# Performance work log

Hardware: AMD Instinct MI355X
Metric: run time of the kernel (lower is better)

## Reference

```python
import jax, jax.numpy as jnp
import numpy as np

N = 1_000_000   # gaussians
K_NB = 10       # neighbor control points per gaussian
K_TOTAL = 300   # num_fine control points


def _normalize(q, eps=1e-8):
    return q / jnp.maximum(jnp.linalg.norm(q, axis=-1, keepdims=True), eps)


def quaternion_to_rotation_matrix(q):
    # q: [..., 4] in (w, x, y, z); normalized before conversion
    q = _normalize(q)
    w, x, y, z = q[..., 0], q[..., 1], q[..., 2], q[..., 3]
    R = jnp.stack([
        jnp.stack([1 - 2 * (y * y + z * z), 2 * (x * y - w * z), 2 * (x * z + w * y)], axis=-1),
        jnp.stack([2 * (x * y + w * z), 1 - 2 * (x * x + z * z), 2 * (y * z - w * x)], axis=-1),
        jnp.stack([2 * (x * z - w * y), 2 * (y * z + w * x), 1 - 2 * (x * x + y * y)], axis=-1),
    ], axis=-2)  # [..., 3, 3]
    return R


def quaternion_multiply(a, b):
    # Hamilton product, (w, x, y, z)
    aw, ax, ay, az = a[..., 0], a[..., 1], a[..., 2], a[..., 3]
    bw, bx, by, bz = b[..., 0], b[..., 1], b[..., 2], b[..., 3]
    return jnp.stack([
        aw * bw - ax * bx - ay * by - az * bz,
        aw * bx + ax * bw + ay * bz - az * by,
        aw * by - ax * bz + ay * bw + az * bx,
        aw * bz + ax * by - ay * bx + az * bw,
    ], axis=-1)


def setup_inputs() -> dict:
    key = jax.random.key(0)
    ks = jax.random.split(key, 7)
    means = jax.random.normal(ks[0], (N, 3), dtype=jnp.float32)
    quaternions = _normalize(jax.random.normal(ks[1], (N, 4), dtype=jnp.float32))
    w = jax.random.uniform(ks[2], (N, K_NB), dtype=jnp.float32) + 1e-3
    weights = w / w.sum(-1, keepdims=True)  # blending weights sum to 1
    indices = jax.random.randint(ks[3], (N, K_NB), 0, K_TOTAL)
    ctrl_translations = 0.1 * jax.random.normal(ks[4], (K_TOTAL, 3), dtype=jnp.float32)
    ctrl_rotations = _normalize(jax.random.normal(ks[5], (K_TOTAL, 4), dtype=jnp.float32))
    ctrl_positions = jax.random.normal(ks[6], (K_TOTAL, 3), dtype=jnp.float32)
    return {
        'means': means, 'quaternions': quaternions, 'weights': weights,
        'ctrl_translations': ctrl_translations, 'ctrl_rotations': ctrl_rotations,
        'ctrl_positions': ctrl_positions, 'indices': indices,
    }


def reference(means, quaternions, weights, ctrl_translations, ctrl_rotations, ctrl_positions, indices):
    # gather neighbor control-point transforms
    nb_trans = ctrl_translations[indices]   # [N, K, 3]
    nb_rots = ctrl_rotations[indices]       # [N, K, 4]
    nb_pos = ctrl_positions[indices]        # [N, K, 3]

    diff = means[:, None, :] - nb_pos                       # [N, K, 3]
    R_ctrl = quaternion_to_rotation_matrix(nb_rots)         # [N, K, 3, 3]
    rotated_diff = jnp.einsum('nkij,nkj->nki', R_ctrl, diff)
    deformed_per_cp = rotated_diff + nb_pos + nb_trans      # [N, K, 3]

    w = weights[..., None]                                  # [N, K, 1]
    deformed_means = (w * deformed_per_cp).sum(axis=1)      # [N, 3]

    blended_rot = _normalize((w * nb_rots).sum(axis=1))     # [N, 4]
    deformed_quats = quaternion_multiply(blended_rot, quaternions)
    return deformed_means, deformed_quats
```

## Files before the change

kernel.cpp:

```cpp
#include <hip/hip_runtime.h>
#include <math.h>


__device__ __forceinline__ void compute_cp(
    const float* __restrict__ ctrl_trans,
    const float* __restrict__ ctrl_rot,
    const float* __restrict__ ctrl_pos,
    int cp, float4* q_out, float4* b_out)
{
    float qw = ctrl_rot[cp * 4 + 0];
    float qx = ctrl_rot[cp * 4 + 1];
    float qy = ctrl_rot[cp * 4 + 2];
    float qz = ctrl_rot[cp * 4 + 3];
    float n   = sqrtf(qw * qw + qx * qx + qy * qy + qz * qz);
    float inv = 1.0f / fmaxf(n, 1e-8f);
    float w = qw * inv, x = qx * inv, y = qy * inv, z = qz * inv;
    float R00 = 1.0f - 2.0f * (y * y + z * z);
    float R01 = 2.0f * (x * y - w * z);
    float R02 = 2.0f * (x * z + w * y);
    float R10 = 2.0f * (x * y + w * z);
    float R11 = 1.0f - 2.0f * (x * x + z * z);
    float R12 = 2.0f * (y * z - w * x);
    float R20 = 2.0f * (x * z - w * y);
    float R21 = 2.0f * (y * z + w * x);
    float R22 = 1.0f - 2.0f * (x * x + y * y);
    float px = ctrl_pos[cp * 3 + 0];
    float py = ctrl_pos[cp * 3 + 1];
    float pz = ctrl_pos[cp * 3 + 2];
    float tx = ctrl_trans[cp * 3 + 0];
    float ty = ctrl_trans[cp * 3 + 1];
    float tz = ctrl_trans[cp * 3 + 2];
    *q_out = make_float4(w, x, y, z);
    *b_out = make_float4(px + tx - (R00 * px + R01 * py + R02 * pz),
                         py + ty - (R10 * px + R11 * py + R12 * pz),
                         pz + tz - (R20 * px + R21 * py + R22 * pz),
                         0.0f);
}

__global__ __launch_bounds__(256) void build_table_kernel(
    const float* __restrict__ ctrl_trans,
    const float* __restrict__ ctrl_rot,
    const float* __restrict__ ctrl_pos,
    float4* __restrict__ table, int K_TOTAL)
{
    int cp = blockIdx.x * blockDim.x + threadIdx.x;
    if (cp >= K_TOTAL) return;
    float4 q, b;
    compute_cp(ctrl_trans, ctrl_rot, ctrl_pos, cp, &q, &b);
    table[cp] = q;
    table[K_TOTAL + cp] = b;
}

template <int KNB>
__device__ __forceinline__ void deform_body(
    const float4* __restrict__ s4,
    const float* __restrict__ means,
    const float* __restrict__ quats,
    const float* __restrict__ weights,
    const int*   __restrict__ indices,
    float* __restrict__ out_means,
    float* __restrict__ out_quats,
    int i, int K_TOTAL, int K_NB_rt)
{
    const int kn = (KNB > 0) ? KNB : K_NB_rt;
    const int*   idx_row = indices + (long long)i * kn;
    const float* w_row   = weights + (long long)i * kn;

    float W = 0.0f;
    float Mxx = 0.0f, Myy = 0.0f, Mzz = 0.0f;
    float Mxy = 0.0f, Mxz = 0.0f, Myz = 0.0f;
    float Mwx = 0.0f, Mwy = 0.0f, Mwz = 0.0f;
    float qsw = 0.0f, qsx = 0.0f, qsy = 0.0f, qsz = 0.0f;
    float bsx = 0.0f, bsy = 0.0f, bsz = 0.0f;

#pragma unroll
    for (int k = 0; k < kn; k++) {
        int   cp = idx_row[k];
        float w  = w_row[k];
        float4 q = s4[cp];
        float4 b = s4[K_TOTAL + cp];
        float tw = w * q.x, tx = w * q.y, ty = w * q.z, tz = w * q.w;
        W += w;
        Mxx = fmaf(tx, q.y, Mxx);
        Myy = fmaf(ty, q.z, Myy);
        Mzz = fmaf(tz, q.w, Mzz);
        Mxy = fmaf(tx, q.z, Mxy);
        Mxz = fmaf(tx, q.w, Mxz);
        Myz = fmaf(ty, q.w, Myz);
        Mwx = fmaf(tw, q.y, Mwx);
        Mwy = fmaf(tw, q.z, Mwy);
        Mwz = fmaf(tw, q.w, Mwz);
        qsw += tw; qsx += tx; qsy += ty; qsz += tz;
        bsx = fmaf(w, b.x, bsx);
        bsy = fmaf(w, b.y, bsy);
        bsz = fmaf(w, b.z, bsz);
    }

    float mx = means[i * 3 + 0];
    float my = means[i * 3 + 1];
    float mz = means[i * 3 + 2];

    float A00 = W - 2.0f * (Myy + Mzz);
    float A01 = 2.0f * (Mxy - Mwz);
    float A02 = 2.0f * (Mxz + Mwy);
    float A10 = 2.0f * (Mxy + Mwz);
    float A11 = W - 2.0f * (Mxx + Mzz);
    float A12 = 2.0f * (Myz - Mwx);
    float A20 = 2.0f * (Mxz - Mwy);
    float A21 = 2.0f * (Myz + Mwx);
    float A22 = W - 2.0f * (Mxx + Myy);

    out_means[i * 3 + 0] = fmaf(A00, mx, fmaf(A01, my, fmaf(A02, mz, bsx)));
    out_means[i * 3 + 1] = fmaf(A10, mx, fmaf(A11, my, fmaf(A12, mz, bsy)));
    out_means[i * 3 + 2] = fmaf(A20, mx, fmaf(A21, my, fmaf(A22, mz, bsz)));

    float n   = sqrtf(qsw * qsw + qsx * qsx + qsy * qsy + qsz * qsz);
    float inv = 1.0f / fmaxf(n, 1e-8f);
    float bw = qsw * inv, bx = qsx * inv, by = qsy * inv, bz = qsz * inv;

    float4 g = ((const float4*)quats)[i];
    float gw = g.x, gx = g.y, gy = g.z, gz = g.w;

    float ow = bw * gw - bx * gx - by * gy - bz * gz;
    float ox = bw * gx + bx * gw + by * gz - bz * gy;
    float oy = bw * gy - bx * gz + by * gw + bz * gx;
    float oz = bw * gz + bx * gy - by * gx + bz * gw;

    float4* oq = (float4*)(out_quats + (long long)i * 4);
    *oq = make_float4(ow, ox, oy, oz);
}

template <int KNB>
__global__ __launch_bounds__(256) void deform_kernel(
    const float* __restrict__ means,
    const float* __restrict__ quats,
    const float* __restrict__ weights,
    const float4* __restrict__ table,
    const int*   __restrict__ indices,
    float* __restrict__ out_means,
    float* __restrict__ out_quats,
    int N, int K_TOTAL, int K_NB_rt)
{
    extern __shared__ float4 s4[];
    int nelem = 2 * K_TOTAL;
    for (int t = threadIdx.x; t < nelem; t += blockDim.x) s4[t] = table[t];
    __syncthreads();

    int i = blockIdx.x * blockDim.x + threadIdx.x;
    if (i >= N) return;
    deform_body<KNB>(s4, means, quats, weights, indices, out_means, out_quats,
                     i, K_TOTAL, K_NB_rt);
}

template <int KNB>
__global__ __launch_bounds__(256) void deform_fused_kernel(
    const float* __restrict__ means,
    const float* __restrict__ quats,
    const float* __restrict__ weights,
    const float* __restrict__ ctrl_trans,
    const float* __restrict__ ctrl_rot,
    const float* __restrict__ ctrl_pos,
    const int*   __restrict__ indices,
    float* __restrict__ out_means,
    float* __restrict__ out_quats,
    int N, int K_TOTAL, int K_NB_rt)
{
    extern __shared__ float4 s4[];
    for (int cp = threadIdx.x; cp < K_TOTAL; cp += blockDim.x) {
        float4 q, b;
        compute_cp(ctrl_trans, ctrl_rot, ctrl_pos, cp, &q, &b);
        s4[cp] = q;
        s4[K_TOTAL + cp] = b;
    }
    __syncthreads();

    int i = blockIdx.x * blockDim.x + threadIdx.x;
    if (i >= N) return;
    deform_body<KNB>(s4, means, quats, weights, indices, out_means, out_quats,
                     i, K_TOTAL, K_NB_rt);
}

extern "C" void kernel_launch(void* const* d_in, const int* in_sizes, int n_in,
                              void* d_out, int out_size, void* d_ws, size_t ws_size,
                              hipStream_t stream) {
    const float* means      = (const float*)d_in[0];
    const float* quats      = (const float*)d_in[1];
    const float* weights    = (const float*)d_in[2];
    const float* ctrl_trans = (const float*)d_in[3];
    const float* ctrl_rot   = (const float*)d_in[4];
    const float* ctrl_pos   = (const float*)d_in[5];
    const int*   indices    = (const int*)d_in[6];

    int N       = in_sizes[0] / 3;
    int K_NB    = in_sizes[2] / N;
    int K_TOTAL = in_sizes[3] / 3;

    float* out_means = (float*)d_out;
    float* out_quats = (float*)d_out + (long long)N * 3;

    int block = 256;
    int grid  = (N + block - 1) / block;
    size_t tbl_bytes = (size_t)K_TOTAL * 2 * sizeof(float4);
    size_t smem = tbl_bytes;

    if (d_ws != nullptr && ws_size >= tbl_bytes) {
        int gb = (K_TOTAL + block - 1) / block;
        build_table_kernel<<<gb, block, 0, stream>>>(
            ctrl_trans, ctrl_rot, ctrl_pos, (float4*)d_ws, K_TOTAL);
        if (K_NB == 10) {
            deform_kernel<10><<<grid, block, smem, stream>>>(
                means, quats, weights, (const float4*)d_ws, indices,
                out_means, out_quats, N, K_TOTAL, K_NB);
        } else {
            deform_kernel<0><<<grid, block, smem, stream>>>(
                means, quats, weights, (const float4*)d_ws, indices,
                out_means, out_quats, N, K_TOTAL, K_NB);
        }
    } else {
        if (K_NB == 10) {
            deform_fused_kernel<10><<<grid, block, smem, stream>>>(
                means, quats, weights, ctrl_trans, ctrl_rot, ctrl_pos, indices,
                out_means, out_quats, N, K_TOTAL, K_NB);
        } else {
            deform_fused_kernel<0><<<grid, block, smem, stream>>>(
                means, quats, weights, ctrl_trans, ctrl_rot, ctrl_pos, indices,
                out_means, out_quats, N, K_TOTAL, K_NB);
        }
    }
}
```

Before: 147.8 us.

## Process two gaussians per thread with vectorized int4/float4 loads and fused table build

Each thread now handles a pair of gaussians, so their 20 indices and 20 weights load as five int4 and five float4 vector loads, and means and outputs use float2 and float4 accesses. The separate table-build kernel is dropped and each block computes the control-point table into shared memory itself. Table entries are interleaved so q and b for one control point sit next to each other. This aims to cut the number of memory transactions and one kernel launch. The cost is redundant per-block table setup, half as many threads in flight, and higher register use.

After: 149.4 us. Within noise of the previous version (+1.1%).

```diff
diff --git a/kernel.cpp b/kernel.cpp
--- a/kernel.cpp
+++ b/kernel.cpp
@@ -37,123 +37,74 @@
                          0.0f);
 }
 
-__global__ __launch_bounds__(256) void build_table_kernel(
-    const float* __restrict__ ctrl_trans,
-    const float* __restrict__ ctrl_rot,
-    const float* __restrict__ ctrl_pos,
-    float4* __restrict__ table, int K_TOTAL)
-{
-    int cp = blockIdx.x * blockDim.x + threadIdx.x;
-    if (cp >= K_TOTAL) return;
-    float4 q, b;
-    compute_cp(ctrl_trans, ctrl_rot, ctrl_pos, cp, &q, &b);
-    table[cp] = q;
-    table[K_TOTAL + cp] = b;
-}
-
-template <int KNB>
-__device__ __forceinline__ void deform_body(
-    const float4* __restrict__ s4,
-    const float* __restrict__ means,
-    const float* __restrict__ quats,
-    const float* __restrict__ weights,
-    const int*   __restrict__ indices,
-    float* __restrict__ out_means,
-    float* __restrict__ out_quats,
-    int i, int K_TOTAL, int K_NB_rt)
-{
-    const int kn = (KNB > 0) ? KNB : K_NB_rt;
-    const int*   idx_row = indices + (long long)i * kn;
-    const float* w_row   = weights + (long long)i * kn;
-
-    float W = 0.0f;
-    float Mxx = 0.0f, Myy = 0.0f, Mzz = 0.0f;
-    float Mxy = 0.0f, Mxz = 0.0f, Myz = 0.0f;
-    float Mwx = 0.0f, Mwy = 0.0f, Mwz = 0.0f;
-    float qsw = 0.0f, qsx = 0.0f, qsy = 0.0f, qsz = 0.0f;
-    float bsx = 0.0f, bsy = 0.0f, bsz = 0.0f;
-
-#pragma unroll
-    for (int k = 0; k < kn; k++) {
-        int   cp = idx_row[k];
-        float w  = w_row[k];
-        float4 q = s4[cp];
-        float4 b = s4[K_TOTAL + cp];
-        float tw = w * q.x, tx = w * q.y, ty = w * q.z, tz = w * q.w;
-        W += w;
-        Mxx = fmaf(tx, q.y, Mxx);
-        Myy = fmaf(ty, q.z, Myy);
-        Mzz = fmaf(tz, q.w, Mzz);
-        Mxy = fmaf(tx, q.z, Mxy);
-        Mxz = fmaf(tx, q.w, Mxz);
-        Myz = fmaf(ty, q.w, Myz);
-        Mwx = fmaf(tw, q.y, Mwx);
-        Mwy = fmaf(tw, q.z, Mwy);
-        Mwz = fmaf(tw, q.w, Mwz);
-        qsw += tw; qsx += tx; qsy += ty; qsz += tz;
-        bsx = fmaf(w, b.x, bsx);
-        bsy = fmaf(w, b.y, bsy);
-        bsz = fmaf(w, b.z, bsz);
-    }
-
-    float mx = means[i * 3 + 0];
-    float my = means[i * 3 + 1];
-    float mz = means[i * 3 + 2];
-
-    float A00 = W - 2.0f * (Myy + Mzz);
-    float A01 = 2.0f * (Mxy - Mwz);
-    float A02 = 2.0f * (Mxz + Mwy);
-    float A10 = 2.0f * (Mxy + Mwz);
-    float A11 = W - 2.0f * (Mxx + Mzz);
-    float A12 = 2.0f * (Myz - Mwx);
-    float A20 = 2.0f * (Mxz - Mwy);
-    float A21 = 2.0f * (Myz + Mwx);
-    float A22 = W - 2.0f * (Mxx + Myy);
-
-    out_means[i * 3 + 0] = fmaf(A00, mx, fmaf(A01, my, fmaf(A02, mz, bsx)));
-    out_means[i * 3 + 1] = fmaf(A10, mx, fmaf(A11, my, fmaf(A12, mz, bsy)));
-    out_means[i * 3 + 2] = fmaf(A20, mx, fmaf(A21, my, fmaf(A22, mz, bsz)));
-
-    float n   = sqrtf(qsw * qsw + qsx * qsx + qsy * qsy + qsz * qsz);
+struct Accum {
+    float W;
+    float Mxx, Myy, Mzz, Mxy, Mxz, Myz, Mwx, Mwy, Mwz;
+    float qsw, qsx, qsy, qsz;
+    float bsx, bsy, bsz;
+};
+
+__device__ __forceinline__ void acc_init(Accum& a) {
+    a.W = 0.0f;
+    a.Mxx = a.Myy = a.Mzz = 0.0f;
+    a.Mxy = a.Mxz = a.Myz = 0.0f;
+    a.Mwx = a.Mwy = a.Mwz = 0.0f;
+    a.qsw = a.qsx = a.qsy = a.qsz = 0.0f;
+    a.bsx = a.bsy = a.bsz = 0.0f;
+}
+
+__device__ __forceinline__ void acc_neighbor(Accum& a, const float4* __restrict__ s4,
+                                             int cp, float w) {
+    float4 q = s4[2 * cp];
+    float4 b = s4[2 * cp + 1];
+    float tw = w * q.x, tx = w * q.y, ty = w * q.z, tz = w * q.w;
+    a.W += w;
+    a.Mxx = fmaf(tx, q.y, a.Mxx);
+    a.Myy = fmaf(ty, q.z, a.Myy);
+    a.Mzz = fmaf(tz, q.w, a.Mzz);
+    a.Mxy = fmaf(tx, q.z, a.Mxy);
+    a.Mxz = fmaf(tx, q.w, a.Mxz);
+    a.Myz = fmaf(ty, q.w, a.Myz);
+    a.Mwx = fmaf(tw, q.y, a.Mwx);
+    a.Mwy = fmaf(tw, q.z, a.Mwy);
+    a.Mwz = fmaf(tw, q.w, a.Mwz);
+    a.qsw += tw; a.qsx += tx; a.qsy += ty; a.qsz += tz;
+    a.bsx = fmaf(w, b.x, a.bsx);
+    a.bsy = fmaf(w, b.y, a.bsy);
+    a.bsz = fmaf(w, b.z, a.bsz);
+}
+
+__device__ __forceinline__ void acc_epilogue(const Accum& a,
+                                             float mx, float my, float mz,
+                                             float4 g,
+                                             float* dmx, float* dmy, float* dmz,
+                                             float4* oq) {
+    float A00 = a.W - 2.0f * (a.Myy + a.Mzz);
+    float A01 = 2.0f * (a.Mxy - a.Mwz);
+    float A02 = 2.0f * (a.Mxz + a.Mwy);
+    float A10 = 2.0f * (a.Mxy + a.Mwz);
+    float A11 = a.W - 2.0f * (a.Mxx + a.Mzz);
+    float A12 = 2.0f * (a.Myz - a.Mwx);
+    float A20 = 2.0f * (a.Mxz - a.Mwy);
+    float A21 = 2.0f * (a.Myz + a.Mwx);
+    float A22 = a.W - 2.0f * (a.Mxx + a.Myy);
+
+    *dmx = fmaf(A00, mx, fmaf(A01, my, fmaf(A02, mz, a.bsx)));
+    *dmy = fmaf(A10, mx, fmaf(A11, my, fmaf(A12, mz, a.bsy)));
+    *dmz = fmaf(A20, mx, fmaf(A21, my, fmaf(A22, mz, a.bsz)));
+
+    float n   = sqrtf(a.qsw * a.qsw + a.qsx * a.qsx + a.qsy * a.qsy + a.qsz * a.qsz);
     float inv = 1.0f / fmaxf(n, 1e-8f);
-    float bw = qsw * inv, bx = qsx * inv, by = qsy * inv, bz = qsz * inv;
-
-    float4 g = ((const float4*)quats)[i];
+    float bw = a.qsw * inv, bx = a.qsx * inv, by = a.qsy * inv, bz = a.qsz * inv;
+
     float gw = g.x, gx = g.y, gy = g.z, gz = g.w;
-
-    float ow = bw * gw - bx * gx - by * gy - bz * gz;
-    float ox = bw * gx + bx * gw + by * gz - bz * gy;
-    float oy = bw * gy - bx * gz + by * gw + bz * gx;
-    float oz = bw * gz + bx * gy - by * gx + bz * gw;
-
-    float4* oq = (float4*)(out_quats + (long long)i * 4);
-    *oq = make_float4(ow, ox, oy, oz);
-}
-
-template <int KNB>
-__global__ __launch_bounds__(256) void deform_kernel(
-    const float* __restrict__ means,
-    const float* __restrict__ quats,
-    const float* __restrict__ weights,
-    const float4* __restrict__ table,
-    const int*   __restrict__ indices,
-    float* __restrict__ out_means,
-    float* __restrict__ out_quats,
-    int N, int K_TOTAL, int K_NB_rt)
-{
-    extern __shared__ float4 s4[];
-    int nelem = 2 * K_TOTAL;
-    for (int t = threadIdx.x; t < nelem; t += blockDim.x) s4[t] = table[t];
-    __syncthreads();
-
-    int i = blockIdx.x * blockDim.x + threadIdx.x;
-    if (i >= N) return;
-    deform_body<KNB>(s4, means, quats, weights, indices, out_means, out_quats,
-                     i, K_TOTAL, K_NB_rt);
-}
-
-template <int KNB>
-__global__ __launch_bounds__(256) void deform_fused_kernel(
+    oq->x = bw * gw - bx * gx - by * gy - bz * gz;
+    oq->y = bw * gx + bx * gw + by * gz - bz * gy;
+    oq->z = bw * gy - bx * gz + by * gw + bz * gx;
+    oq->w = bw * gz + bx * gy - by * gx + bz * gw;
+}
+
+__global__ __launch_bounds__(256) void deform_pair_kernel(
     const float* __restrict__ means,
     const float* __restrict__ quats,
     const float* __restrict__ weights,
@@ -163,21 +114,133 @@
     const int*   __restrict__ indices,
     float* __restrict__ out_means,
     float* __restrict__ out_quats,
-    int N, int K_TOTAL, int K_NB_rt)
+    int N, int K_TOTAL)
 {
     extern __shared__ float4 s4[];
     for (int cp = threadIdx.x; cp < K_TOTAL; cp += blockDim.x) {
         float4 q, b;
         compute_cp(ctrl_trans, ctrl_rot, ctrl_pos, cp, &q, &b);
-        s4[cp] = q;
-        s4[K_TOTAL + cp] = b;
+        s4[2 * cp]     = q;
+        s4[2 * cp + 1] = b;
     }
     __syncthreads();
 
-    int i = blockIdx.x * blockDim.x + threadIdx.x;
+    long long tid = (long long)blockIdx.x * blockDim.x + threadIdx.x;
+    long long i0  = 2 * tid;
+    if (i0 >= N) return;
+
+    if (i0 + 1 < N) {
+        const int4*   ip = (const int4*)(indices + i0 * 10);
+        const float4* wp = (const float4*)(weights + i0 * 10);
+        int4   I0 = ip[0], I1 = ip[1], I2 = ip[2], I3 = ip[3], I4 = ip[4];
+        float4 W0 = wp[0], W1 = wp[1], W2 = wp[2], W3 = wp[3], W4 = wp[4];
+
+        Accum a0; acc_init(a0);
+        acc_neighbor(a0, s4, I0.x, W0.x);
+        acc_neighbor(a0, s4, I0.y, W0.y);
+        acc_neighbor(a0, s4, I0.z, W0.z);
+        acc_neighbor(a0, s4, I0.w, W0.w);
+        acc_neighbor(a0, s4, I1.x, W1.x);
+        acc_neighbor(a0, s4, I1.y, W1.y);
+        acc_neighbor(a0, s4, I1.z, W1.z);
+        acc_neighbor(a0, s4, I1.w, W1.w);
+        acc_neighbor(a0, s4, I2.x, W2.x);
+        acc_neighbor(a0, s4, I2.y, W2.y);
+
+        Accum a1; acc_init(a1);
+        acc_neighbor(a1, s4, I2.z, W2.z);
+        acc_neighbor(a1, s4, I2.w, W2.w);
+        acc_neighbor(a1, s4, I3.x, W3.x);
+        acc_neighbor(a1, s4, I3.y, W3.y);
+        acc_neighbor(a1, s4, I3.z, W3.z);
+        acc_neighbor(a1, s4, I3.w, W3.w);
+        acc_neighbor(a1, s4, I4.x, W4.x);
+        acc_neighbor(a1, s4, I4.y, W4.y);
+        acc_neighbor(a1, s4, I4.z, W4.z);
+        acc_neighbor(a1, s4, I4.w, W4.w);
+
+        const float2* mp = (const float2*)(means + i0 * 3);
+        float2 m01 = mp[0], m23 = mp[1], m45 = mp[2];
+
+        float4 g0 = ((const float4*)quats)[i0];
+        float4 g1 = ((const float4*)quats)[i0 + 1];
+
+        float d0x, d0y, d0z, d1x, d1y, d1z;
+        float4 oq0, oq1;
+        acc_epilogue(a0, m01.x, m01.y, m23.x, g0, &d0x, &d0y, &d0z, &oq0);
+        acc_epilogue(a1, m23.y, m45.x, m45.y, g1, &d1x, &d1y, &d1z, &oq1);
+
+        float2* omp = (float2*)(out_means + i0 * 3);
+        omp[0] = make_float2(d0x, d0y);
+        omp[1] = make_float2(d0z, d1x);
+        omp[2] = make_float2(d1y, d1z);
+
+        float4* oqp = (float4*)(out_quats + i0 * 4);
+        oqp[0] = oq0;
+        oqp[1] = oq1;
+    } else {
+        const int*   idx_row = indices + i0 * 10;
+        const float* w_row   = weights + i0 * 10;
+        Accum a0; acc_init(a0);
+#pragma unroll
+        for (int k = 0; k < 10; k++)
+            acc_neighbor(a0, s4, idx_row[k], w_row[k]);
+
+        float mx = means[i0 * 3 + 0];
+        float my = means[i0 * 3 + 1];
+        float mz = means[i0 * 3 + 2];
+        float4 g0 = ((const float4*)quats)[i0];
+        float dx, dy, dz;
+        float4 oq0;
+        acc_epilogue(a0, mx, my, mz, g0, &dx, &dy, &dz, &oq0);
+        out_means[i0 * 3 + 0] = dx;
+        out_means[i0 * 3 + 1] = dy;
+        out_means[i0 * 3 + 2] = dz;
+        ((float4*)out_quats)[i0] = oq0;
+    }
+}
+
+__global__ __launch_bounds__(256) void deform_generic_kernel(
+    const float* __restrict__ means,
+    const float* __restrict__ quats,
+    const float* __restrict__ weights,
+    const float* __restrict__ ctrl_trans,
+    const float* __restrict__ ctrl_rot,
+    const float* __restrict__ ctrl_pos,
+    const int*   __restrict__ indices,
+    float* __restrict__ out_means,
+    float* __restrict__ out_quats,
+    int N, int K_NB, int K_TOTAL)
+{
+    extern __shared__ float4 s4[];
+    for (int cp = threadIdx.x; cp < K_TOTAL; cp += blockDim.x) {
+        float4 q, b;
+        compute_cp(ctrl_trans, ctrl_rot, ctrl_pos, cp, &q, &b);
+        s4[2 * cp]     = q;
+        s4[2 * cp + 1] = b;
+    }
+    __syncthreads();
+
+    long long i = (long long)blockIdx.x * blockDim.x + threadIdx.x;
     if (i >= N) return;
-    deform_body<KNB>(s4, means, quats, weights, indices, out_means, out_quats,
-                     i, K_TOTAL, K_NB_rt);
+
+    const int*   idx_row = indices + i * K_NB;
+    const float* w_row   = weights + i * K_NB;
+    Accum a0; acc_init(a0);
+    for (int k = 0; k < K_NB; k++)
+        acc_neighbor(a0, s4, idx_row[k], w_row[k]);
+
+    float mx = means[i * 3 + 0];
+    float my = means[i * 3 + 1];
+    float mz = means[i * 3 + 2];
+    float4 g0 = ((const float4*)quats)[i];
+    float dx, dy, dz;
+    float4 oq0;
+    acc_epilogue(a0, mx, my, mz, g0, &dx, &dy, &dz, &oq0);
+    out_means[i * 3 + 0] = dx;
+    out_means[i * 3 + 1] = dy;
+    out_means[i * 3 + 2] = dz;
+    ((float4*)out_quats)[i] = oq0;
 }
 
 extern "C" void kernel_launch(void* const* d_in, const int* in_sizes, int n_in,
@@ -199,32 +262,18 @@
     float* out_quats = (float*)d_out + (long long)N * 3;
 
     int block = 256;
-    int grid  = (N + block - 1) / block;
-    size_t tbl_bytes = (size_t)K_TOTAL * 2 * sizeof(float4);
-    size_t smem = tbl_bytes;
-
-    if (d_ws != nullptr && ws_size >= tbl_bytes) {
-        int gb = (K_TOTAL + block - 1) / block;
-        build_table_kernel<<<gb, block, 0, stream>>>(
-            ctrl_trans, ctrl_rot, ctrl_pos, (float4*)d_ws, K_TOTAL);
-        if (K_NB == 10) {
-            deform_kernel<10><<<grid, block, smem, stream>>>(
-                means, quats, weights, (const float4*)d_ws, indices,
-                out_means, out_quats, N, K_TOTAL, K_NB);
-        } else {
-            deform_kernel<0><<<grid, block, smem, stream>>>(
-                means, quats, weights, (const float4*)d_ws, indices,
-                out_means, out_quats, N, K_TOTAL, K_NB);
-        }
+    size_t smem = (size_t)K_TOTAL * 2 * sizeof(float4);
+
+    if (K_NB == 10) {
+        long long pairs = ((long long)N + 1) / 2;
+        int grid = (int)((pairs + block - 1) / block);
+        deform_pair_kernel<<<grid, block, smem, stream>>>(
+            means, quats, weights, ctrl_trans, ctrl_rot, ctrl_pos, indices,
+            out_means, out_quats, N, K_TOTAL);
     } else {
-        if (K_NB == 10) {
-            deform_fused_kernel<10><<<grid, block, smem, stream>>>(
-                means, quats, weights, ctrl_trans, ctrl_rot, ctrl_pos, indices,
-                out_means, out_quats, N, K_TOTAL, K_NB);
-        } else {
-            deform_fused_kernel<0><<<grid, block, smem, stream>>>(
-                means, quats, weights, ctrl_trans, ctrl_rot, ctrl_pos, indices,
-                out_means, out_quats, N, K_TOTAL, K_NB);
-        }
-    }
-}
+        int grid = (int)(((long long)N + block - 1) / block);
+        deform_generic_kernel<<<grid, block, smem, stream>>>(
+            means, quats, weights, ctrl_trans, ctrl_rot, ctrl_pos, indices,
+            out_means, out_quats, N, K_NB, K_TOTAL);
+    }
+}
```
